# Performance work log

Hardware: AMD Instinct MI355X
Metric: run time of the kernel (lower is better)

Reference implementation:

```python
import jax, jax.numpy as jnp
import numpy as np

N = 4096
D_IN = 512
D_OUT = 512

def setup_inputs() -> dict:
    key = jax.random.key(0)
    k1, k2, k3 = jax.random.split(key, 3)
    X = jax.random.normal(k1, (N, D_IN), dtype=jnp.float32)
    A = jax.random.uniform(k2, (N, N), dtype=jnp.float32)
    # Linear(input_dim, output_dim, bias=False): W is [out, in], y = x @ W.T
    W = jax.random.normal(k3, (D_OUT, D_IN), dtype=jnp.float32) * (1.0 / np.sqrt(D_IN))
    return {"X": X, "A": A, "W": W}

def reference(X, A, W):
    # A2 = A + I
    A2 = A + jnp.eye(A.shape[0], dtype=A.dtype)
    # Dhat = diag(diagonal(A2)); fractional_matrix_power(Dhat, -1/2) on a
    # diagonal matrix is elementwise d^{-1/2}; dense diag GEMMs reduce to
    # row/column scaling.
    dscale = jnp.diagonal(A2) ** (-0.5)  # [N]
    temp = (A2 @ X) @ W.T                # [N, D_OUT]
    A_norm = dscale[:, None] * A2 * dscale[None, :]  # D^-1/2 A2 D^-1/2
    return jax.nn.relu(A_norm @ temp)
```

## Files before the change

kernel.cpp:

```cpp
#include <hip/hip_runtime.h>
#include <hip/hip_bf16.h>
#include <stdint.h>

typedef float  f32x4  __attribute__((ext_vector_type(4)));
typedef __bf16 bf16x8 __attribute__((ext_vector_type(8)));
typedef unsigned short us4 __attribute__((ext_vector_type(4)));

#define NDIM 4096
#define DDIM 512

__device__ __forceinline__ unsigned short f2bf(float f) {
    union { float f; uint32_t u; } v; v.f = f;
    uint32_t u = v.u;
    u += 0x7FFFu + ((u >> 16) & 1u);
    return (unsigned short)(u >> 16);
}

__global__ void prep_kernel(const float* __restrict__ A, const float* __restrict__ X,
                            const float* __restrict__ W,
                            unsigned short* __restrict__ A2, unsigned short* __restrict__ Xb,
                            unsigned short* __restrict__ Wb, float* __restrict__ ds) {
    const int b = blockIdx.x, tid = threadIdx.x;
    if (b < 16384) {
        int i = b * 256 + tid;
        int e = i << 2;
        int row = e >> 12, col = e & 4095;
        f32x4 v = ((const f32x4*)A)[i];
        int d = row - col;
        if (d >= 0 && d < 4) v[d] += 1.0f;
        us4 o; o.x = f2bf(v.x); o.y = f2bf(v.y); o.z = f2bf(v.z); o.w = f2bf(v.w);
        ((us4*)A2)[i] = o;
    } else if (b < 18432) {
        int i = (b - 16384) * 256 + tid;
        f32x4 v = ((const f32x4*)X)[i];
        us4 o; o.x = f2bf(v.x); o.y = f2bf(v.y); o.z = f2bf(v.z); o.w = f2bf(v.w);
        ((us4*)Xb)[i] = o;
    } else if (b < 18688) {
        int i = (b - 18432) * 256 + tid;
        f32x4 v = ((const f32x4*)W)[i];
        us4 o; o.x = f2bf(v.x); o.y = f2bf(v.y); o.z = f2bf(v.z); o.w = f2bf(v.w);
        ((us4*)Wb)[i] = o;
    } else {
        int i = (b - 18688) * 256 + tid;
        if (i < NDIM) ds[i] = rsqrtf(A[(size_t)i * (NDIM + 1)] + 1.0f);
    }
}

template <int MODE>
__global__ __launch_bounds__(256, 2) void gemm_bt(
    const unsigned short* __restrict__ A,
    const unsigned short* __restrict__ B,
    void* __restrict__ C,
    const float* __restrict__ ds,
    int K, int ldc)
{
    __shared__ unsigned short lsA[64 * 64];
    __shared__ unsigned short lsB[64 * 64];

    const int tid  = threadIdx.x;
    const int wid  = tid >> 6;
    const int lane = tid & 63;
    const int m0 = blockIdx.x * 64;
    const int n0 = blockIdx.y * 64;
    const int wm = (wid & 1) * 32;
    const int wn = (wid >> 1) * 32;

    const int lrow = lane >> 3;
    const int lcsw = ((lane & 7) ^ lrow) * 16;

    f32x4 acc[2][2];
    #pragma unroll
    for (int i = 0; i < 2; i++)
        #pragma unroll
        for (int j = 0; j < 2; j++) acc[i][j] = (f32x4)0.0f;

    const char* gA = (const char*)A + ((size_t)(m0 + wid * 16 + lrow) * K) * 2 + lcsw;
    const char* gB = (const char*)B + ((size_t)(n0 + wid * 16 + lrow) * K) * 2 + lcsw;
    const size_t rowstep = (size_t)8 * K * 2;

    for (int k0 = 0; k0 < K; k0 += 64) {
        const size_t kb = (size_t)k0 * 2;
        #pragma unroll
        for (int i = 0; i < 2; i++) {
            __builtin_amdgcn_global_load_lds(
                (const __attribute__((address_space(1))) void*)(gA + kb + (size_t)i * rowstep),
                (__attribute__((address_space(3))) void*)(&lsA[(wid * 2 + i) * 512]),
                16, 0, 0);
            __builtin_amdgcn_global_load_lds(
                (const __attribute__((address_space(1))) void*)(gB + kb + (size_t)i * rowstep),
                (__attribute__((address_space(3))) void*)(&lsB[(wid * 2 + i) * 512]),
                16, 0, 0);
        }
        __syncthreads();

        #pragma unroll
        for (int ks = 0; ks < 2; ks++) {
            const int kboff = ks * 64 + (lane >> 4) * 16;
            bf16x8 bfrag[2], afrag[2];
            #pragma unroll
            for (int nt = 0; nt < 2; nt++) {
                int r = wn + nt * 16 + (lane & 15);
                bfrag[nt] = *(const bf16x8*)((const char*)lsB + r * 128 + (kboff ^ ((r & 7) * 16)));
            }
            #pragma unroll
            for (int mt = 0; mt < 2; mt++) {
                int r = wm + mt * 16 + (lane & 15);
                afrag[mt] = *(const bf16x8*)((const char*)lsA + r * 128 + (kboff ^ ((r & 7) * 16)));
            }
            #pragma unroll
            for (int mt = 0; mt < 2; mt++)
                #pragma unroll
                for (int nt = 0; nt < 2; nt++)
                    acc[mt][nt] = __builtin_amdgcn_mfma_f32_16x16x32_bf16(
                        afrag[mt], bfrag[nt], acc[mt][nt], 0, 0, 0);
        }
        __syncthreads();
    }

    const int col  = lane & 15;
    const int quad = lane >> 4;
    #pragma unroll
    for (int mt = 0; mt < 2; mt++) {
        const int gm0 = m0 + wm + mt * 16 + quad * 4;
        f32x4 d;
        if (MODE >= 1) d = *(const f32x4*)(ds + gm0);
        else           d = (f32x4)1.0f;
        #pragma unroll
        for (int nt = 0; nt < 2; nt++) {
            const int gn = n0 + wn + nt * 16 + col;
            f32x4 v = acc[mt][nt];
            if (MODE <= 1) {
                us4 o;
                o.x = f2bf(v.x * d.x);
                o.y = f2bf(v.y * d.y);
                o.z = f2bf(v.z * d.z);
                o.w = f2bf(v.w * d.w);
                *(us4*)((unsigned short*)C + (size_t)gn * ldc + gm0) = o;
            } else {
                float* o = (float*)C + (size_t)gm0 * ldc + gn;
                o[0]               = fmaxf(v.x * d.x, 0.0f);
                o[ldc]             = fmaxf(v.y * d.y, 0.0f);
                o[2 * (size_t)ldc] = fmaxf(v.z * d.z, 0.0f);
                o[3 * (size_t)ldc] = fmaxf(v.w * d.w, 0.0f);
            }
        }
    }
}

extern "C" void kernel_launch(void* const* d_in, const int* in_sizes, int n_in,
                              void* d_out, int out_size, void* d_ws, size_t ws_size,
                              hipStream_t stream) {
    const float* X = (const float*)d_in[0];
    const float* A = (const float*)d_in[1];
    const float* W = (const float*)d_in[2];

    char* ws = (char*)d_ws;
    float*          dsc = (float*)ws;
    unsigned short* A2  = (unsigned short*)(ws + (16u << 10));
    unsigned short* Xb  = (unsigned short*)(ws + (16u << 10) + 33554432u);
    unsigned short* Wb  = (unsigned short*)(ws + (16u << 10) + 33554432u + 4194304u);
    unsigned short* Yt  = (unsigned short*)(ws + (16u << 10) + 33554432u + 4194304u + 524288u);
    unsigned short* T2  = (unsigned short*)(ws + (16u << 10) + 33554432u + 4194304u + 524288u + 4194304u);

    prep_kernel<<<18704, 256, 0, stream>>>(A, X, W, A2, Xb, Wb, dsc);

    dim3 grid(64, 8), blk(256);
    gemm_bt<0><<<grid, blk, 0, stream>>>(Xb, Wb, Yt, nullptr, 512, 4096);
    gemm_bt<1><<<grid, blk, 0, stream>>>(A2, Yt, T2, dsc, 4096, 4096);
    gemm_bt<2><<<grid, blk, 0, stream>>>(A2, T2, d_out, dsc, 4096, 512);
}
```

Measured before the change: 195.3 us.

## Split-K the two large GEMMs with atomic fp32 accumulation and separate epilogues

The two N×N-by-N×D GEMMs switch to split-K over four K chunks, with the grid's z dimension picking the chunk. Partial sums go into a zeroed fp32 scratch buffer through atomic adds, and separate elementwise kernels apply the D^-1/2 scaling, the bf16 conversion or ReLU, and re-zero the buffer. The second GEMM now computes the transposed product directly, using swapped operands and a swapped block mapping. The goal is more blocks in flight and higher occupancy (launch bounds raised to 8), at the cost of atomic traffic, extra scratch reads and writes, and two more launches.

```diff
diff --git a/kernel.cpp b/kernel.cpp
--- a/kernel.cpp
+++ b/kernel.cpp
@@ -19,7 +19,8 @@
 __global__ void prep_kernel(const float* __restrict__ A, const float* __restrict__ X,
                             const float* __restrict__ W,
                             unsigned short* __restrict__ A2, unsigned short* __restrict__ Xb,
-                            unsigned short* __restrict__ Wb, float* __restrict__ ds) {
+                            unsigned short* __restrict__ Wb, float* __restrict__ ds,
+                            float* __restrict__ Ctmp) {
     const int b = blockIdx.x, tid = threadIdx.x;
     if (b < 16384) {
         int i = b * 256 + tid;
@@ -40,19 +41,21 @@
         f32x4 v = ((const f32x4*)W)[i];
         us4 o; o.x = f2bf(v.x); o.y = f2bf(v.y); o.z = f2bf(v.z); o.w = f2bf(v.w);
         ((us4*)Wb)[i] = o;
-    } else {
+    } else if (b < 18704) {
         int i = (b - 18688) * 256 + tid;
         if (i < NDIM) ds[i] = rsqrtf(A[(size_t)i * (NDIM + 1)] + 1.0f);
+    } else {
+        int i = (b - 18704) * 256 + tid;
+        ((f32x4*)Ctmp)[i] = (f32x4)0.0f;
     }
 }
 
-template <int MODE>
-__global__ __launch_bounds__(256, 2) void gemm_bt(
+template <int MODE, int SWAP>
+__global__ __launch_bounds__(256, 8) void gemm_bt(
     const unsigned short* __restrict__ A,
     const unsigned short* __restrict__ B,
     void* __restrict__ C,
-    const float* __restrict__ ds,
-    int K, int ldc)
+    int K, int kc, int ldc)
 {
     __shared__ unsigned short lsA[64 * 64];
     __shared__ unsigned short lsB[64 * 64];
@@ -60,8 +63,9 @@
     const int tid  = threadIdx.x;
     const int wid  = tid >> 6;
     const int lane = tid & 63;
-    const int m0 = blockIdx.x * 64;
-    const int n0 = blockIdx.y * 64;
+    const int m0 = (SWAP ? blockIdx.y : blockIdx.x) * 64;
+    const int n0 = (SWAP ? blockIdx.x : blockIdx.y) * 64;
+    const int kbase = blockIdx.z * kc;
     const int wm = (wid & 1) * 32;
     const int wn = (wid >> 1) * 32;
 
@@ -78,7 +82,7 @@
     const char* gB = (const char*)B + ((size_t)(n0 + wid * 16 + lrow) * K) * 2 + lcsw;
     const size_t rowstep = (size_t)8 * K * 2;
 
-    for (int k0 = 0; k0 < K; k0 += 64) {
+    for (int k0 = kbase; k0 < kbase + kc; k0 += 64) {
         const size_t kb = (size_t)k0 * 2;
         #pragma unroll
         for (int i = 0; i < 2; i++) {
@@ -122,29 +126,50 @@
     #pragma unroll
     for (int mt = 0; mt < 2; mt++) {
         const int gm0 = m0 + wm + mt * 16 + quad * 4;
-        f32x4 d;
-        if (MODE >= 1) d = *(const f32x4*)(ds + gm0);
-        else           d = (f32x4)1.0f;
         #pragma unroll
         for (int nt = 0; nt < 2; nt++) {
             const int gn = n0 + wn + nt * 16 + col;
             f32x4 v = acc[mt][nt];
-            if (MODE <= 1) {
+            if (MODE == 0) {
                 us4 o;
-                o.x = f2bf(v.x * d.x);
-                o.y = f2bf(v.y * d.y);
-                o.z = f2bf(v.z * d.z);
-                o.w = f2bf(v.w * d.w);
+                o.x = f2bf(v.x); o.y = f2bf(v.y); o.z = f2bf(v.z); o.w = f2bf(v.w);
                 *(us4*)((unsigned short*)C + (size_t)gn * ldc + gm0) = o;
             } else {
                 float* o = (float*)C + (size_t)gm0 * ldc + gn;
-                o[0]               = fmaxf(v.x * d.x, 0.0f);
-                o[ldc]             = fmaxf(v.y * d.y, 0.0f);
-                o[2 * (size_t)ldc] = fmaxf(v.z * d.z, 0.0f);
-                o[3 * (size_t)ldc] = fmaxf(v.w * d.w, 0.0f);
+                unsafeAtomicAdd(&o[0],               v.x);
+                unsafeAtomicAdd(&o[ldc],             v.y);
+                unsafeAtomicAdd(&o[2 * (size_t)ldc], v.z);
+                unsafeAtomicAdd(&o[3 * (size_t)ldc], v.w);
             }
         }
     }
+}
+
+__global__ void ep2_kernel(float* __restrict__ Ctmp, const float* __restrict__ ds,
+                           unsigned short* __restrict__ T2) {
+    int t = blockIdx.x * 256 + threadIdx.x;
+    int e = t << 2;
+    int i = e & 4095;
+    f32x4 v = ((f32x4*)Ctmp)[t];
+    f32x4 d = *(const f32x4*)(ds + i);
+    us4 o;
+    o.x = f2bf(v.x * d.x); o.y = f2bf(v.y * d.y);
+    o.z = f2bf(v.z * d.z); o.w = f2bf(v.w * d.w);
+    ((us4*)T2)[t] = o;
+    ((f32x4*)Ctmp)[t] = (f32x4)0.0f;
+}
+
+__global__ void ep3_kernel(const float* __restrict__ Ctmp, const float* __restrict__ ds,
+                           float* __restrict__ out) {
+    int t = blockIdx.x * 256 + threadIdx.x;
+    int e = t << 2;
+    int i = e >> 9;
+    float s = ds[i];
+    f32x4 v = ((const f32x4*)Ctmp)[t];
+    f32x4 o;
+    o.x = fmaxf(v.x * s, 0.0f); o.y = fmaxf(v.y * s, 0.0f);
+    o.z = fmaxf(v.z * s, 0.0f); o.w = fmaxf(v.w * s, 0.0f);
+    ((f32x4*)out)[t] = o;
 }
 
 extern "C" void kernel_launch(void* const* d_in, const int* in_sizes, int n_in,
@@ -155,17 +180,19 @@
     const float* W = (const float*)d_in[2];
 
     char* ws = (char*)d_ws;
-    float*          dsc = (float*)ws;
-    unsigned short* A2  = (unsigned short*)(ws + (16u << 10));
-    unsigned short* Xb  = (unsigned short*)(ws + (16u << 10) + 33554432u);
-    unsigned short* Wb  = (unsigned short*)(ws + (16u << 10) + 33554432u + 4194304u);
-    unsigned short* Yt  = (unsigned short*)(ws + (16u << 10) + 33554432u + 4194304u + 524288u);
-    unsigned short* T2  = (unsigned short*)(ws + (16u << 10) + 33554432u + 4194304u + 524288u + 4194304u);
+    float*          dsc  = (float*)ws;
+    unsigned short* A2   = (unsigned short*)(ws + 16384);
+    unsigned short* Xb   = (unsigned short*)(ws + 33570816u);
+    unsigned short* Wb   = (unsigned short*)(ws + 37765120u);
+    unsigned short* Yt   = (unsigned short*)(ws + 38289408u);
+    unsigned short* T2   = (unsigned short*)(ws + 42483712u);
+    float*          Ctmp = (float*)(ws + 46678016u);
 
-    prep_kernel<<<18704, 256, 0, stream>>>(A, X, W, A2, Xb, Wb, dsc);
+    prep_kernel<<<20752, 256, 0, stream>>>(A, X, W, A2, Xb, Wb, dsc, Ctmp);
 
-    dim3 grid(64, 8), blk(256);
-    gemm_bt<0><<<grid, blk, 0, stream>>>(Xb, Wb, Yt, nullptr, 512, 4096);
-    gemm_bt<1><<<grid, blk, 0, stream>>>(A2, Yt, T2, dsc, 4096, 4096);
-    gemm_bt<2><<<grid, blk, 0, stream>>>(A2, T2, d_out, dsc, 4096, 512);
+    gemm_bt<0, 0><<<dim3(64, 8, 1), 256, 0, stream>>>(Xb, Wb, Yt, 512, 512, 4096);
+    gemm_bt<3, 1><<<dim3(64, 8, 4), 256, 0, stream>>>(Yt, A2, Ctmp, 4096, 1024, 4096);
+    ep2_kernel<<<2048, 256, 0, stream>>>(Ctmp, dsc, T2);
+    gemm_bt<3, 0><<<dim3(64, 8, 4), 256, 0, stream>>>(A2, T2, Ctmp, 4096, 1024, 512);
+    ep3_kernel<<<2048, 256, 0, stream>>>(Ctmp, dsc, (float*)d_out);
 }
```

After: 207.6 us. +6.3%, slower.
